# Kernel tuning notes

Hardware: AMD Instinct MI355X
Metric: run time of the kernel (lower is better)

## Reference

```python
import jax, jax.numpy as jnp
import numpy as np
from jax import lax

EPS = 1e-8
DN = ('NCHW', 'OIHW', 'NCHW')


def setup_inputs() -> dict:
    key = jax.random.key(0)
    k1, k2 = jax.random.split(key)
    inputs = jax.random.normal(k1, (16, 3, 512, 512), dtype=jnp.float32)
    template = jax.random.normal(k2, (16, 3, 21, 21), dtype=jnp.float32)
    return {"inputs": inputs, "template": template}


def _normalize_template(template):
    # Z-normalize each (batch, channel) plane independently, then divide by
    # patch element count (matches NCC.__init__).
    B, C, th, tw = template.shape
    t = template.reshape(B, C, th * tw)
    t = t - jnp.mean(t, axis=-1, keepdims=True)
    t = t / (jnp.std(t, axis=-1, keepdims=True) + EPS)  # ddof=0 == unbiased=False
    return t.reshape(B, C, th, tw) / (th * tw)


def reference(inputs, template):
    B, C, H, W = inputs.shape
    th, tw = template.shape[2], template.shape[3]
    nt = _normalize_template(template)

    # Per-(b,c) depthwise cross-correlation (the grouped conv with eye-masked
    # weights is exactly a depthwise conv with per-sample filters).
    x = inputs.reshape(1, B * C, H, W)
    w = nt.reshape(B * C, 1, th, tw)
    res = lax.conv_general_dilated(x, w, (1, 1), 'VALID',
                                   dimension_numbers=DN,
                                   feature_group_count=B * C)
    res = res.reshape(B, C, res.shape[2], res.shape[3])  # (B,C,Hout,Wout)

    # Local (patch) std per channel via box filter (shared across batch).
    box = jnp.full((C, 1, th, tw), 1.0 / (th * tw), dtype=inputs.dtype)
    mean = lax.conv_general_dilated(inputs, box, (1, 1), 'VALID',
                                    dimension_numbers=DN, feature_group_count=C)
    mean_sq = lax.conv_general_dilated(inputs * inputs, box, (1, 1), 'VALID',
                                       dimension_numbers=DN, feature_group_count=C)
    std = jnp.sqrt(mean_sq - mean * mean + EPS)

    return res / (std + EPS)
```

## Files before the change

kernel.cpp:

```cpp
#include <hip/hip_runtime.h>
#include <math.h>

typedef __attribute__((ext_vector_type(8)))  short short8;
typedef __attribute__((ext_vector_type(16))) float f32x16;

#define NPLANE 48
#define H 512
#define W 512
#define TH 21
#define OH 492
#define OW 492
#define EPSF 1e-8f

#define STRIDE 168
#define SEG_ROWS 84

#define BONES_HOFF (4128768u / 2)

__device__ inline unsigned short f2bf(float f) {
    unsigned u = __float_as_uint(f);
    return (unsigned short)((u + 0x7FFFu + ((u >> 16) & 1u)) >> 16);
}
__device__ inline float bf2f(unsigned s) {
    return __uint_as_float(s << 16);
}

#if defined(__has_builtin)
#if __has_builtin(__builtin_amdgcn_cvt_pk_bf16_f32)
#define HAVE_CVT_PK_BF16 1
#endif
#endif

#ifdef HAVE_CVT_PK_BF16
typedef __attribute__((ext_vector_type(2))) __bf16 bf16x2;
__device__ inline unsigned pack2bf(float a, float b) {
    bf16x2 r = __builtin_amdgcn_cvt_pk_bf16_f32(a, b);
    return *(unsigned*)&r;
}
#else
__device__ inline unsigned pack2bf(float a, float b) {
    return (unsigned)f2bf(a) | ((unsigned)f2bf(b) << 16);
}
#endif

__global__ void build_b_kernel(const float* __restrict__ tpl,
                               unsigned short* __restrict__ ws16) {
    __shared__ float sm[2];
    const int plane = blockIdx.x;
    const float* t = tpl + plane * 441;
    const int tid = threadIdx.x;
    if (tid < 64) {
        float s = 0.f, s2 = 0.f;
        for (int k = tid; k < 441; k += 64) {
            float x = t[k];
            s += x; s2 += x * x;
        }
#pragma unroll
        for (int o = 32; o >= 1; o >>= 1) {
            s  += __shfl_down(s, o);
            s2 += __shfl_down(s2, o);
        }
        if (tid == 0) {
            float mean = s / 441.f;
            float var = fmaxf(s2 / 441.f - mean * mean, 0.f);
            sm[0] = mean;
            sm[1] = 1.f / ((sqrtf(var) + EPSF) * 441.f);
        }
    }
    __syncthreads();
    const float mean = sm[0], scale = sm[1];

    unsigned short* bc = ws16 + (size_t)plane * 43008;
    for (int i = tid; i < 43008; i += 256) {
        int j = i & 7, lane = (i >> 3) & 63, s = (i >> 9) & 3, u = i >> 11;
        int k = ((lane >> 5) << 3) + j, n = lane & 31;
        int v = 16 * s + k - n;
        float val = (v >= 0 && v < TH) ? (t[u * 21 + v] - mean) * scale : 0.f;
        bc[i] = f2bf(val);
    }
    if (plane == 0) {
        unsigned short* bo = ws16 + BONES_HOFF;
        const unsigned short one = f2bf(1.f);
        for (int i = tid; i < 2048; i += 256) {
            int j = i & 7, lane = (i >> 3) & 63, s = (i >> 9) & 3;
            int k = ((lane >> 5) << 3) + j, n = lane & 31;
            int v = 16 * s + k - n;
            bo[i] = (v >= 0 && v < TH) ? one : (unsigned short)0;
        }
    }
}

__global__ __launch_bounds__(256, 3) void ncc_fused_kernel(
    const float* __restrict__ in, const unsigned short* __restrict__ ws16,
    float* __restrict__ out) {
    __shared__ short seg[SEG_ROWS * STRIDE];
    __shared__ short vbuf[64 * STRIDE];

    const int plane = blockIdx.z;
    const int x0 = blockIdx.x * 128;
    const int y0 = blockIdx.y * 64;
    const int tid = threadIdx.x;
    const int lane = tid & 63;
    const int tr = (tid >> 6) & 1;
    const int tc = tid >> 7;
    const float* src = in + (size_t)plane * H * W;

    for (int i = tid; i < SEG_ROWS * 20; i += 256) {
        int row = i / 20, s8 = i - row * 20;
        int gy = y0 + row, gx = x0 + s8 * 8;
        if (gy < H && gx + 7 < W) {
            float4 a = *(const float4*)(src + gy * W + gx);
            float4 b = *(const float4*)(src + gy * W + gx + 4);
            int4 p;
            p.x = (int)pack2bf(a.x, a.y);
            p.y = (int)pack2bf(a.z, a.w);
            p.z = (int)pack2bf(b.x, b.y);
            p.w = (int)pack2bf(b.z, b.w);
            *(int4*)&seg[row * STRIDE + s8 * 8] = p;
        } else {
            short8 val;
#pragma unroll
            for (int e = 0; e < 8; ++e) {
                float xv = (gy < H && gx + e < W) ? src[gy * W + gx + e] : 0.f;
                val[e] = (short)f2bf(xv);
            }
            *(short8*)&seg[row * STRIDE + s8 * 8] = val;
        }
    }
    __syncthreads();

    const int m = lane & 31;
    const int half = lane >> 5;
    const int abase = (tr * 32 + m) * STRIDE + tc * 64 + half * 8;
    const unsigned short* bc = ws16 + (size_t)plane * 43008 + lane * 8;

    const unsigned short* bo16 = ws16 + BONES_HOFF + lane * 8;
    short8 bones[4];
#pragma unroll
    for (int s = 0; s < 4; ++s)
        bones[s] = *(const short8*)(bo16 + s * 512);

    f32x16 acc[2];
#pragma unroll
    for (int t = 0; t < 2; ++t)
#pragma unroll
        for (int e = 0; e < 16; ++e) acc[t][e] = 0.f;

#pragma unroll
    for (int u = 0; u < TH; ++u) {
        short8 bf[4];
#pragma unroll
        for (int s = 0; s < 4; ++s)
            bf[s] = *(const short8*)(bc + (u * 4 + s) * 512);
        short8 af[6];
#pragma unroll
        for (int g = 0; g < 6; ++g)
            af[g] = *(const short8*)&seg[abase + u * STRIDE + g * 16];
#pragma unroll
        for (int t = 0; t < 2; ++t)
#pragma unroll
            for (int s = 0; s < 4; ++s)
                acc[t] = __builtin_amdgcn_mfma_f32_32x32x16_bf16(
                    af[2 * t + s], bf[s], acc[t], 0, 0, 0);
    }
    __syncthreads();

    if (tid < 80) {
        const int c2 = tid * 2;
        float s0 = 0.f, s1 = 0.f, q0 = 0.f, q1 = 0.f;
#pragma unroll
        for (int r = 0; r < 20; ++r) {
            unsigned p = *(const unsigned*)&seg[r * STRIDE + c2];
            float a = bf2f(p & 0xffffu), b = bf2f(p >> 16);
            s0 += a; s1 += b;
            q0 = fmaf(a, a, q0); q1 = fmaf(b, b, q1);
        }
        for (int y = 0; y < 64; ++y) {
            unsigned p = *(const unsigned*)&seg[(y + 20) * STRIDE + c2];
            float a = bf2f(p & 0xffffu), b = bf2f(p >> 16);
            s0 += a; s1 += b;
            q0 = fmaf(a, a, q0); q1 = fmaf(b, b, q1);
            *(unsigned*)&vbuf[y * STRIDE + c2] = pack2bf(s0, s1);
            unsigned o = *(const unsigned*)&seg[y * STRIDE + c2];
            float c = bf2f(o & 0xffffu), d = bf2f(o >> 16);
            *(unsigned*)&seg[y * STRIDE + c2] = pack2bf(q0, q1);
            s0 -= c; s1 -= d;
            q0 = fmaf(-c, c, q0); q1 = fmaf(-d, d, q1);
        }
    }
    __syncthreads();

    const float invn = 1.f / 441.f;
    float* outp = out + (size_t)plane * OH * OW;
#pragma unroll
    for (int t = 0; t < 2; ++t) {
        f32x16 aS, aQ;
#pragma unroll
        for (int e = 0; e < 16; ++e) { aS[e] = 0.f; aQ[e] = 0.f; }
#pragma unroll
        for (int s = 0; s < 4; ++s) {
            short8 vf = *(const short8*)&vbuf[abase + (2 * t + s) * 16];
            aS = __builtin_amdgcn_mfma_f32_32x32x16_bf16(vf, bones[s], aS,
                                                         0, 0, 0);
            short8 qf = *(const short8*)&seg[abase + (2 * t + s) * 16];
            aQ = __builtin_amdgcn_mfma_f32_32x32x16_bf16(qf, bones[s], aQ,
                                                         0, 0, 0);
        }
        const int gx = x0 + tc * 64 + t * 32 + (lane & 31);
        if (gx < OW) {
#pragma unroll
            for (int r = 0; r < 16; ++r) {
                int gy = y0 + tr * 32 + (r & 3) + ((r >> 2) << 3) + half * 4;
                if (gy < OH) {
                    float mean = aS[r] * invn;
                    float msq = aQ[r] * invn;
                    float sd =
                        __builtin_amdgcn_sqrtf(msq - mean * mean + EPSF);
                    outp[(size_t)gy * OW + gx] =
                        acc[t][r] * __builtin_amdgcn_rcpf(sd + EPSF);
                }
            }
        }
    }
}

extern "C" void kernel_launch(void* const* d_in, const int* in_sizes, int n_in,
                              void* d_out, int out_size, void* d_ws,
                              size_t ws_size, hipStream_t stream) {
    const float* inputs = (const float*)d_in[0];
    const float* tmpl = (const float*)d_in[1];
    float* out = (float*)d_out;
    unsigned short* ws16 = (unsigned short*)d_ws;

    build_b_kernel<<<NPLANE, 256, 0, stream>>>(tmpl, ws16);
    ncc_fused_kernel<<<dim3(4, 8, NPLANE), 256, 0, stream>>>(inputs, ws16, out);
}
```

Before: 164.1 us.

## Split local-std computation into separate kernel writing fp16 inverse-std map

Moves the box-filter mean/variance computation out of the fused MFMA kernel into a new kernel that computes running column and row sums in fp32/fp16 and writes a per-pixel inverse std as fp16. The MFMA kernel then just multiplies its correlation accumulator by the loaded factor, dropping the vbuf shared buffer and the extra ones-matrix MFMAs, and raises its occupancy hint from 3 to 5 blocks. In exchange it adds a kernel launch, an extra global read of the input and a round trip of the fp16 normalization map. Storing S and Q sums in fp16 also costs precision.

```diff
diff --git a/kernel.cpp b/kernel.cpp
--- a/kernel.cpp
+++ b/kernel.cpp
@@ -1,4 +1,5 @@
 #include <hip/hip_runtime.h>
+#include <hip/hip_fp16.h>
 #include <math.h>
 
 typedef __attribute__((ext_vector_type(8)))  short short8;
@@ -15,14 +16,11 @@
 #define STRIDE 168
 #define SEG_ROWS 84
 
-#define BONES_HOFF (4128768u / 2)
+#define N_HOFF_BYTES 4194304u
 
 __device__ inline unsigned short f2bf(float f) {
     unsigned u = __float_as_uint(f);
     return (unsigned short)((u + 0x7FFFu + ((u >> 16) & 1u)) >> 16);
-}
-__device__ inline float bf2f(unsigned s) {
-    return __uint_as_float(s << 16);
 }
 
 #if defined(__has_builtin)
@@ -78,23 +76,90 @@
         float val = (v >= 0 && v < TH) ? (t[u * 21 + v] - mean) * scale : 0.f;
         bc[i] = f2bf(val);
     }
-    if (plane == 0) {
-        unsigned short* bo = ws16 + BONES_HOFF;
-        const unsigned short one = f2bf(1.f);
-        for (int i = tid; i < 2048; i += 256) {
-            int j = i & 7, lane = (i >> 3) & 63, s = (i >> 9) & 3;
-            int k = ((lane >> 5) << 3) + j, n = lane & 31;
-            int v = 16 * s + k - n;
-            bo[i] = (v >= 0 && v < TH) ? one : (unsigned short)0;
-        }
-    }
-}
-
-__global__ __launch_bounds__(256, 3) void ncc_fused_kernel(
+}
+
+__global__ __launch_bounds__(256, 2) void nstd_kernel(
+    const float* __restrict__ in, __half* __restrict__ N) {
+    __shared__ unsigned vb[64 * 216];
+
+    const int plane = blockIdx.z;
+    const int x0 = blockIdx.x * 192;
+    const int y0 = blockIdx.y * 64;
+    const int tid = threadIdx.x;
+    const float* src = in + (size_t)plane * H * W;
+
+    if (tid < 212) {
+        const int x = x0 + tid;
+        const bool ok = (x < W);
+        float s = 0.f, q = 0.f;
+#pragma unroll
+        for (int r = 0; r < 20; ++r) {
+            float v = ok ? src[(y0 + r) * W + x] : 0.f;
+            s += v;
+            q = fmaf(v, v, q);
+        }
+        for (int i = 0; i < 64; ++i) {
+            int gy = y0 + 20 + i;
+            float v = (ok && gy < H) ? src[gy * W + x] : 0.f;
+            s += v;
+            q = fmaf(v, v, q);
+            __half2 p;
+            p.x = __float2half(s);
+            p.y = __float2half(q);
+            vb[i * 216 + tid] = *(unsigned*)&p;
+            float o = ok ? src[(y0 + i) * W + x] : 0.f;
+            s -= o;
+            q = fmaf(-o, o, q);
+        }
+    }
+    __syncthreads();
+
+    const int row = tid >> 2;
+    const int sg = tid & 3;
+    const int base = row * 216 + sg * 48;
+    const int gy = y0 + row;
+    const float invn = 1.f / 441.f;
+    __half* nrow = N + ((size_t)plane * OH + gy) * OW;
+
+    float S = 0.f, Q = 0.f;
+#pragma unroll
+    for (int k = 0; k < 20; ++k) {
+        __half2 p = *(__half2*)&vb[base + k];
+        S += __half2float(p.x);
+        Q += __half2float(p.y);
+    }
+    float hold = 0.f;
+    for (int j = 0; j < 48; ++j) {
+        __half2 p = *(__half2*)&vb[base + j + 20];
+        S += __half2float(p.x);
+        Q += __half2float(p.y);
+        float mean = S * invn;
+        float msq = Q * invn;
+        float sd = __builtin_amdgcn_sqrtf(msq - mean * mean + EPSF);
+        float inv = __builtin_amdgcn_rcpf(sd + EPSF);
+        int gx = x0 + sg * 48 + j;
+        if ((j & 1) == 0) {
+            hold = inv;
+        } else if (gy < OH) {
+            if (gx < OW) {
+                __half2 o;
+                o.x = __float2half(hold);
+                o.y = __float2half(inv);
+                *(__half2*)&nrow[gx - 1] = o;
+            } else if (gx - 1 < OW) {
+                nrow[gx - 1] = __float2half(hold);
+            }
+        }
+        __half2 d = *(__half2*)&vb[base + j];
+        S -= __half2float(d.x);
+        Q -= __half2float(d.y);
+    }
+}
+
+__global__ __launch_bounds__(256, 5) void ncc_mfma_kernel(
     const float* __restrict__ in, const unsigned short* __restrict__ ws16,
-    float* __restrict__ out) {
+    const __half* __restrict__ N, float* __restrict__ out) {
     __shared__ short seg[SEG_ROWS * STRIDE];
-    __shared__ short vbuf[64 * STRIDE];
 
     const int plane = blockIdx.z;
     const int x0 = blockIdx.x * 128;
@@ -134,12 +199,6 @@
     const int abase = (tr * 32 + m) * STRIDE + tc * 64 + half * 8;
     const unsigned short* bc = ws16 + (size_t)plane * 43008 + lane * 8;
 
-    const unsigned short* bo16 = ws16 + BONES_HOFF + lane * 8;
-    short8 bones[4];
-#pragma unroll
-    for (int s = 0; s < 4; ++s)
-        bones[s] = *(const short8*)(bo16 + s * 512);
-
     f32x16 acc[2];
 #pragma unroll
     for (int t = 0; t < 2; ++t)
@@ -163,61 +222,19 @@
                 acc[t] = __builtin_amdgcn_mfma_f32_32x32x16_bf16(
                     af[2 * t + s], bf[s], acc[t], 0, 0, 0);
     }
-    __syncthreads();
-
-    if (tid < 80) {
-        const int c2 = tid * 2;
-        float s0 = 0.f, s1 = 0.f, q0 = 0.f, q1 = 0.f;
-#pragma unroll
-        for (int r = 0; r < 20; ++r) {
-            unsigned p = *(const unsigned*)&seg[r * STRIDE + c2];
-            float a = bf2f(p & 0xffffu), b = bf2f(p >> 16);
-            s0 += a; s1 += b;
-            q0 = fmaf(a, a, q0); q1 = fmaf(b, b, q1);
-        }
-        for (int y = 0; y < 64; ++y) {
-            unsigned p = *(const unsigned*)&seg[(y + 20) * STRIDE + c2];
-            float a = bf2f(p & 0xffffu), b = bf2f(p >> 16);
-            s0 += a; s1 += b;
-            q0 = fmaf(a, a, q0); q1 = fmaf(b, b, q1);
-            *(unsigned*)&vbuf[y * STRIDE + c2] = pack2bf(s0, s1);
-            unsigned o = *(const unsigned*)&seg[y * STRIDE + c2];
-            float c = bf2f(o & 0xffffu), d = bf2f(o >> 16);
-            *(unsigned*)&seg[y * STRIDE + c2] = pack2bf(q0, q1);
-            s0 -= c; s1 -= d;
-            q0 = fmaf(-c, c, q0); q1 = fmaf(-d, d, q1);
-        }
-    }
-    __syncthreads();
-
-    const float invn = 1.f / 441.f;
+
+    const __half* Np = N + (size_t)plane * OH * OW;
     float* outp = out + (size_t)plane * OH * OW;
 #pragma unroll
     for (int t = 0; t < 2; ++t) {
-        f32x16 aS, aQ;
-#pragma unroll
-        for (int e = 0; e < 16; ++e) { aS[e] = 0.f; aQ[e] = 0.f; }
-#pragma unroll
-        for (int s = 0; s < 4; ++s) {
-            short8 vf = *(const short8*)&vbuf[abase + (2 * t + s) * 16];
-            aS = __builtin_amdgcn_mfma_f32_32x32x16_bf16(vf, bones[s], aS,
-                                                         0, 0, 0);
-            short8 qf = *(const short8*)&seg[abase + (2 * t + s) * 16];
-            aQ = __builtin_amdgcn_mfma_f32_32x32x16_bf16(qf, bones[s], aQ,
-                                                         0, 0, 0);
-        }
         const int gx = x0 + tc * 64 + t * 32 + (lane & 31);
         if (gx < OW) {
 #pragma unroll
             for (int r = 0; r < 16; ++r) {
                 int gy = y0 + tr * 32 + (r & 3) + ((r >> 2) << 3) + half * 4;
                 if (gy < OH) {
-                    float mean = aS[r] * invn;
-                    float msq = aQ[r] * invn;
-                    float sd =
-                        __builtin_amdgcn_sqrtf(msq - mean * mean + EPSF);
-                    outp[(size_t)gy * OW + gx] =
-                        acc[t][r] * __builtin_amdgcn_rcpf(sd + EPSF);
+                    size_t idx = (size_t)gy * OW + gx;
+                    outp[idx] = acc[t][r] * __half2float(Np[idx]);
                 }
             }
         }
@@ -231,7 +248,10 @@
     const float* tmpl = (const float*)d_in[1];
     float* out = (float*)d_out;
     unsigned short* ws16 = (unsigned short*)d_ws;
+    __half* Nbuf = (__half*)((char*)d_ws + N_HOFF_BYTES);
 
     build_b_kernel<<<NPLANE, 256, 0, stream>>>(tmpl, ws16);
-    ncc_fused_kernel<<<dim3(4, 8, NPLANE), 256, 0, stream>>>(inputs, ws16, out);
-}
+    nstd_kernel<<<dim3(3, 8, NPLANE), 256, 0, stream>>>(inputs, Nbuf);
+    ncc_mfma_kernel<<<dim3(4, 8, NPLANE), 256, 0, stream>>>(inputs, ws16, Nbuf,
+                                                            out);
+}
```

Result: slower. 271.3 us (+65.3%).
